# Kernel optimization log

Hardware: AMD Instinct MI355X
Metric: run time of the kernel (lower is better)

The kernel has to match this reference:

```python
import jax, jax.numpy as jnp
import numpy as np

EPS = 1e-8  # torch cosine_similarity norm clamp
TEMP = 1.0

def _gelu(h):
    return jax.nn.gelu(h, approximate=False)  # torch nn.GELU default (erf)

def _layernorm(h, g, b, eps=1e-5):
    mu = jnp.mean(h, axis=-1, keepdims=True)
    var = jnp.var(h, axis=-1, keepdims=True)
    return (h - mu) * jax.lax.rsqrt(var + eps) * g + b

def _encoder(h, eW1, eb1, eW2, eb2, eW3, eb3, ln_g, ln_b):
    h = _gelu(h @ eW1 + eb1)
    h = _gelu(h @ eW2 + eb2)
    h = h @ eW3 + eb3
    return _layernorm(h, ln_g, ln_b)

def _normalize(v):
    n = jnp.sqrt(jnp.sum(v * v, axis=-1, keepdims=True))
    return v / jnp.maximum(n, EPS)

def setup_inputs() -> dict:
    key = jax.random.key(0)
    ks = jax.random.split(key, 8)
    B, D, H, K = 16384, 512, 512, 11
    s = 0.02
    return {
        'x': jax.random.normal(ks[0], (B, D), jnp.float32),
        'tW1': jax.random.normal(ks[1], (K, D, H), jnp.float32) * s,
        'tb1': jnp.zeros((K, H), jnp.float32),
        'tW2': jax.random.normal(ks[2], (K, H, H), jnp.float32) * s,
        'tb2': jnp.zeros((K, H), jnp.float32),
        'tW3': jax.random.normal(ks[3], (K, H, D), jnp.float32) * s,
        'tb3': jnp.zeros((K, D), jnp.float32),
        'eW1': jax.random.normal(ks[4], (D, H), jnp.float32) * s,
        'eb1': jnp.zeros((H,), jnp.float32),
        'eW2': jax.random.normal(ks[5], (H, H), jnp.float32) * s,
        'eb2': jnp.zeros((H,), jnp.float32),
        'eW3': jax.random.normal(ks[6], (H, H), jnp.float32) * s,
        'eb3': jnp.zeros((H,), jnp.float32),
        'ln_g': jnp.ones((H,), jnp.float32),
        'ln_b': jnp.zeros((H,), jnp.float32),
    }

def reference(x, tW1, tb1, tW2, tb2, tW3, tb3, eW1, eb1, eW2, eb2, eW3, eb3, ln_g, ln_b):
    K = tW1.shape[0]
    # K learned transforms, vectorized over k: [K, B, D]
    h = _gelu(jnp.einsum('bi,kij->kbj', x, tW1) + tb1[:, None, :])
    h = _gelu(jnp.einsum('kbi,kij->kbj', h, tW2) + tb2[:, None, :])
    tx = jnp.einsum('kbi,kij->kbj', h, tW3) + tb3[:, None, :]
    # shared encoder on x and on each transformed view
    z = _encoder(x, eW1, eb1, eW2, eb2, eW3, eb3, ln_g, ln_b)      # [B, H]
    zk = _encoder(tx, eW1, eb1, eW2, eb2, eW3, eb3, ln_g, ln_b)    # [K, B, H]
    zn = _normalize(z)
    zkn = _normalize(zk)
    pos = jnp.einsum('bh,kbh->kb', zn, zkn) / TEMP                 # sim(z, z_k)
    S = jnp.einsum('lbh,kbh->lkb', zkn, zkn) / TEMP                # sim(z_l, z_k)
    diag = jnp.eye(K, dtype=bool)[:, :, None]
    Sm = jnp.where(diag, -jnp.inf, S)                              # drop l == k
    all_terms = jnp.concatenate([pos[None], Sm], axis=0)           # [K+1, K, B]
    log_den = jax.nn.logsumexp(all_terms, axis=0)                  # [K, B]
    return -jnp.sum(pos - log_den, axis=0)                         # [B]
```

## Files before the change

### kernel.cpp

```cpp
#include <hip/hip_runtime.h>
#include <hip/hip_bf16.h>
#include <cstdint>

typedef __attribute__((ext_vector_type(8))) short short8;
typedef __attribute__((ext_vector_type(4))) float f32x4;
typedef __attribute__((ext_vector_type(4))) short short4v;

__device__ __forceinline__ float b2f(short s) {
    unsigned u = ((unsigned)(unsigned short)s) << 16;
    return __builtin_bit_cast(float, u);
}
__device__ __forceinline__ short f2b(float f) {
    unsigned u = __builtin_bit_cast(unsigned, f);
    u += 0x7fff + ((u >> 16) & 1);
    return (short)(u >> 16);
}

__device__ __forceinline__ float gelu_t(float x) {
    const float c1 = 2.302184829f;
    const float c2 = 0.102947246f;
    float x2 = x * x;
    float t  = __builtin_fmaf(c2, x2, c1);
    float e  = __builtin_amdgcn_exp2f(x * t);
    return x - __fdividef(x, e + 1.0f);
}

__device__ __forceinline__ void async16(const void* g, void* l) {
    __builtin_amdgcn_global_load_lds(
        (const __attribute__((address_space(1))) unsigned int*)g,
        (__attribute__((address_space(3))) unsigned int*)l, 16, 0, 0);
}

#define NT 8

template<bool GELU>
__global__ __launch_bounds__(512, 2)
void gemm_bt(const short* __restrict__ A, long sA,
             const short* __restrict__ Bt, long sB,
             const float* __restrict__ bias, long sBias,
             short* __restrict__ C, long sC) {
    const int z = blockIdx.z;
    A    += (long)z * sA;
    Bt   += (long)z * sB;
    bias += (long)z * sBias;
    C    += (long)z * sC;

    const int nwg = (int)gridDim.x;
    const int bx  = (int)blockIdx.x;
    int flat = bx;
    if ((nwg & 7) == 0) { const int q = nwg >> 3; flat = (bx & 7) * q + (bx >> 3); }
    const long arow0 = (long)(flat >> 1) * 256;
    const long brow0 = (long)(flat & 1) * 256;

    __shared__ alignas(16) short smem[2 * 2 * 256 * 64];

    const int tid  = threadIdx.x;
    const int lane = tid & 63;
    const int w    = tid >> 6;
    const int wrow = w >> 2, wcol = w & 3;
    const int lr = lane & 15, hi = lane >> 4;

    f32x4 acc[8][4] = {};

    const int srow = lane >> 3;
    const int sc   = ((lane & 7) ^ srow) * 8;

    auto stage = [&](int q, int t) {
        short* Ab = smem + q * 32768;
        short* Bb = Ab + 16384;
        const int k0 = t * 64;
#pragma unroll
        for (int j = 0; j < 4; ++j) {
            const int rbase = j * 64 + w * 8;
            async16(A  + (arow0 + rbase + srow) * 512 + k0 + sc, Ab + rbase * 64);
            async16(Bt + (brow0 + rbase + srow) * 512 + k0 + sc, Bb + rbase * 64);
        }
    };

    stage(0, 0);

    int buf = 0;
#pragma unroll
    for (int t = 0; t < NT; ++t) {
        if (t + 1 < NT) {
            stage(buf ^ 1, t + 1);
            asm volatile("s_waitcnt vmcnt(8)" ::: "memory");
        } else {
            asm volatile("s_waitcnt vmcnt(0)" ::: "memory");
        }
        __builtin_amdgcn_sched_barrier(0);
        __builtin_amdgcn_s_barrier();
        __builtin_amdgcn_sched_barrier(0);

        const short* Ab = smem + buf * 32768;
        const short* Bb = Ab + 16384;
#pragma unroll
        for (int ks = 0; ks < 2; ++ks) {
            const int ch = ks * 4 + hi;
            short8 a[8], b[4];
#pragma unroll
            for (int n = 0; n < 4; ++n) {
                const int r = wcol * 64 + n * 16 + lr;
                b[n] = *(const short8*)&Bb[r * 64 + ((ch ^ (r & 7)) * 8)];
            }
#pragma unroll
            for (int m = 0; m < 8; ++m) {
                const int r = wrow * 128 + m * 16 + lr;
                a[m] = *(const short8*)&Ab[r * 64 + ((ch ^ (r & 7)) * 8)];
            }
            __builtin_amdgcn_s_setprio(1);
#pragma unroll
            for (int m = 0; m < 8; ++m)
#pragma unroll
                for (int n = 0; n < 4; ++n)
                    acc[m][n] = __builtin_amdgcn_mfma_f32_16x16x32_bf16(
                        a[m], b[n], acc[m][n], 0, 0, 0);
            __builtin_amdgcn_s_setprio(0);
        }

        __builtin_amdgcn_s_barrier();
        buf ^= 1;
    }

    short* E = smem + w * (32 * 72);
    const int cl = lr, rl = hi * 4;
#pragma unroll
    for (int h = 0; h < 4; ++h) {
#pragma unroll
        for (int n = 0; n < 4; ++n) {
            const int col = (int)brow0 + wcol * 64 + n * 16 + cl;
            const float bs = bias[col];
            const int ecol = n * 16 + cl;
#pragma unroll
            for (int ml = 0; ml < 2; ++ml) {
                const int m = h * 2 + ml;
                float g0 = acc[m][n][0] + bs, g1 = acc[m][n][1] + bs;
                float g2 = acc[m][n][2] + bs, g3 = acc[m][n][3] + bs;
                if (GELU) { g0 = gelu_t(g0); g1 = gelu_t(g1); g2 = gelu_t(g2); g3 = gelu_t(g3); }
                unsigned p01, p23;
                asm("v_cvt_pk_bf16_f32 %0, %1, %2" : "=v"(p01) : "v"(g0), "v"(g1));
                asm("v_cvt_pk_bf16_f32 %0, %1, %2" : "=v"(p23) : "v"(g2), "v"(g3));
                const int r0 = ml * 16 + rl;
                E[(r0 + 0) * 72 + ecol] = (short)(p01 & 0xffff);
                E[(r0 + 1) * 72 + ecol] = (short)(p01 >> 16);
                E[(r0 + 2) * 72 + ecol] = (short)(p23 & 0xffff);
                E[(r0 + 3) * 72 + ecol] = (short)(p23 >> 16);
            }
        }
#pragma unroll
        for (int chunk = 0; chunk < 4; ++chunk) {
            const int rloc = chunk * 8 + (lane >> 3);
            const int c0   = (lane & 7) * 8;
            short8 v = *(const short8*)&E[rloc * 72 + c0];
            *(short8*)&C[(arow0 + wrow * 128 + h * 32 + rloc) * 512
                         + brow0 + wcol * 64 + c0] = v;
        }
    }
}

__global__ __launch_bounds__(256)
void transpose_conv(const float* __restrict__ src, short* __restrict__ dst) {
    __shared__ float t[32][33];
    const long moff = (long)blockIdx.z * 512 * 512;
    const float* s = src + moff;
    short* d = dst + moff;
    const int tx = threadIdx.x & 31, ty = threadIdx.x >> 5;
    const int bi = blockIdx.x, bj = blockIdx.y;
#pragma unroll
    for (int j = 0; j < 4; ++j)
        t[ty + j * 8][tx] = s[(long)(bi * 32 + ty + j * 8) * 512 + bj * 32 + tx];
    __syncthreads();
#pragma unroll
    for (int j = 0; j < 4; ++j)
        d[(long)(bj * 32 + ty + j * 8) * 512 + bi * 32 + tx] = f2b(t[tx][ty + j * 8]);
}

__global__ __launch_bounds__(256)
void conv_f32_bf16_2(const float* __restrict__ src, short* __restrict__ d1,
                     short* __restrict__ d2, long n) {
    long i = ((long)blockIdx.x * 256 + threadIdx.x) * 4;
    if (i >= n) return;
    float4 f = *(const float4*)&src[i];
    short4v o;
    o[0] = f2b(f.x); o[1] = f2b(f.y); o[2] = f2b(f.z); o[3] = f2b(f.w);
    *(short4v*)&d1[i] = o;
    *(short4v*)&d2[i] = o;
}

__global__ __launch_bounds__(256)
void ln_loss(const short* __restrict__ H, const float* __restrict__ g,
             const float* __restrict__ bta, float* __restrict__ out, int CH) {
    __shared__ alignas(16) short Z[4][16 * 520];
    const int wid = threadIdx.x >> 6, lane = threadIdx.x & 63;
    const long b = (long)blockIdx.x * 4 + wid;
    short* Zw = &Z[wid][0];

#pragma unroll
    for (int r = 12; r < 16; ++r)
        *(short8*)&Zw[r * 520 + lane * 8] = (short8){0, 0, 0, 0, 0, 0, 0, 0};

    for (int s = 0; s < 12; ++s) {
        short8 t = *(const short8*)&H[((long)s * CH + b) * 512 + lane * 8];
        float v[8];
        float sum = 0.f, ss = 0.f;
#pragma unroll
        for (int j = 0; j < 8; ++j) { v[j] = b2f(t[j]); sum += v[j]; ss += v[j] * v[j]; }
#pragma unroll
        for (int o = 1; o < 64; o <<= 1) { sum += __shfl_xor(sum, o, 64); ss += __shfl_xor(ss, o, 64); }
        const float mu = sum * (1.f / 512.f);
        const float rs = rsqrtf(ss * (1.f / 512.f) - mu * mu + 1e-5f);
        float y[8]; float nsq = 0.f;
#pragma unroll
        for (int j = 0; j < 8; ++j) {
            const int col = lane * 8 + j;
            y[j] = (v[j] - mu) * rs * g[col] + bta[col];
            nsq += y[j] * y[j];
        }
#pragma unroll
        for (int o = 1; o < 64; o <<= 1) nsq += __shfl_xor(nsq, o, 64);
        const float inv = 1.f / fmaxf(sqrtf(nsq), 1e-8f);
        short8 o8;
#pragma unroll
        for (int j = 0; j < 8; ++j) o8[j] = f2b(y[j] * inv);
        *(short8*)&Zw[s * 520 + lane * 8] = o8;
    }

    f32x4 acc = {0.f, 0.f, 0.f, 0.f};
    const int lr = lane & 15, hi = lane >> 4;
#pragma unroll
    for (int st = 0; st < 16; ++st) {
        short8 a = *(const short8*)&Zw[lr * 520 + st * 32 + hi * 8];
        acc = __builtin_amdgcn_mfma_f32_16x16x32_bf16(a, a, acc, 0, 0, 0);
    }
    const int col = lr;
    float lmax = -3.0e38f;
    bool valid[4];
#pragma unroll
    for (int i = 0; i < 4; ++i) {
        const int row = hi * 4 + i;
        valid[i] = (row < 12) && (row != col);
        if (valid[i]) lmax = fmaxf(lmax, acc[i]);
    }
    lmax = fmaxf(lmax, __shfl_xor(lmax, 16, 64));
    lmax = fmaxf(lmax, __shfl_xor(lmax, 32, 64));
    float esum = 0.f;
#pragma unroll
    for (int i = 0; i < 4; ++i)
        if (valid[i]) esum += __builtin_amdgcn_exp2f((acc[i] - lmax) * 1.44269504f);
    esum += __shfl_xor(esum, 16, 64);
    esum += __shfl_xor(esum, 32, 64);
    float contrib = 0.f;
    if (hi == 0 && col >= 1 && col <= 11) {
        const float logden = lmax + __builtin_amdgcn_logf(esum) * 0.6931471806f;
        contrib = acc[0] - logden;
    }
#pragma unroll
    for (int o = 1; o < 16; o <<= 1) contrib += __shfl_xor(contrib, o, 64);
    if (lane == 0) out[b] = -contrib;
}

extern "C" void kernel_launch(void* const* d_in, const int* in_sizes, int n_in,
                              void* d_out, int out_size, void* d_ws, size_t ws_size,
                              hipStream_t stream) {
    const float* x    = (const float*)d_in[0];
    const float* tW1  = (const float*)d_in[1];
    const float* tb1  = (const float*)d_in[2];
    const float* tW2  = (const float*)d_in[3];
    const float* tb2  = (const float*)d_in[4];
    const float* tW3  = (const float*)d_in[5];
    const float* tb3  = (const float*)d_in[6];
    const float* eW1  = (const float*)d_in[7];
    const float* eb1  = (const float*)d_in[8];
    const float* eW2  = (const float*)d_in[9];
    const float* eb2  = (const float*)d_in[10];
    const float* eW3  = (const float*)d_in[11];
    const float* eb3  = (const float*)d_in[12];
    const float* ln_g = (const float*)d_in[13];
    const float* ln_b = (const float*)d_in[14];

    const int  B    = in_sizes[0] / 512;
    const long WMAT = 512L * 512L;

    int  c  = 1;
    long CH = B;
    for (;;) {
        CH = (long)B / c;
        size_t need = (size_t)36 * WMAT * 2 + (size_t)24 * CH * 512 * 2 + 4096;
        if (need <= ws_size || CH <= 256) break;
        c <<= 1;
    }
    const long SLAB = 12L * CH * 512;

    short* wt  = (short*)d_ws;
    short* X12 = wt  + 36L * WMAT;
    short* hA  = X12 + SLAB;

    {
        dim3 tgK(16, 16, 11), tg1(16, 16, 1);
        transpose_conv<<<tgK, 256, 0, stream>>>(tW1, wt + 0L * WMAT);
        transpose_conv<<<tgK, 256, 0, stream>>>(tW2, wt + 11L * WMAT);
        transpose_conv<<<tgK, 256, 0, stream>>>(tW3, wt + 22L * WMAT);
        transpose_conv<<<tg1, 256, 0, stream>>>(eW1, wt + 33L * WMAT);
        transpose_conv<<<tg1, 256, 0, stream>>>(eW2, wt + 34L * WMAT);
        transpose_conv<<<tg1, 256, 0, stream>>>(eW3, wt + 35L * WMAT);
    }

    const long SC = CH * 512;
    const dim3 gT((unsigned)(CH / 256 * 2), 1, 11);
    const dim3 gE((unsigned)(12 * CH / 256 * 2), 1, 1);

    for (int ch = 0; ch < c; ++ch) {
        conv_f32_bf16_2<<<(unsigned)((SC / 4 + 255) / 256), 256, 0, stream>>>(
            x + (long)ch * SC, X12, hA, SC);

        gemm_bt<true ><<<gT, 512, 0, stream>>>(hA,        0,  wt + 0L * WMAT,  WMAT, tb1, 512, X12 + SC, SC);
        gemm_bt<true ><<<gT, 512, 0, stream>>>(X12 + SC,  SC, wt + 11L * WMAT, WMAT, tb2, 512, hA + SC,  SC);
        gemm_bt<false><<<gT, 512, 0, stream>>>(hA + SC,   SC, wt + 22L * WMAT, WMAT, tb3, 512, X12 + SC, SC);

        gemm_bt<true ><<<gE, 512, 0, stream>>>(X12, 0, wt + 33L * WMAT, 0, eb1, 0, hA,  0);
        gemm_bt<true ><<<gE, 512, 0, stream>>>(hA,  0, wt + 34L * WMAT, 0, eb2, 0, X12, 0);
        gemm_bt<false><<<gE, 512, 0, stream>>>(X12, 0, wt + 35L * WMAT, 0, eb3, 0, hA,  0);

        ln_loss<<<(unsigned)(CH / 4), 256, 0, stream>>>(
            hA, ln_g, ln_b, (float*)d_out + (long)ch * CH, (int)CH);
    }
}
```

Before: 1.001 ms.

## Fold transform layer-3 weights into encoder first layer to drop a GEMM

Precomputes the products tW3[k]·eW1 (and folded biases tb3·eW1+eb1) once per call, so the third transform GEMM and the first encoder GEMM merge into one batched GEMM over 12 slices. The x slice uses eW1 directly, with a zero-stride first-row arrangement. This removes one full B×512×512×12 GEMM pass and its intermediate traffic, at the cost of small setup GEMMs and extra bf16 rounding of the fused weight matrices.

Measured after the change: 911.2 us. 8.9% less time.

```diff
diff --git a/kernel.cpp b/kernel.cpp
--- a/kernel.cpp
+++ b/kernel.cpp
@@ -176,15 +176,29 @@
 }
 
 __global__ __launch_bounds__(256)
-void conv_f32_bf16_2(const float* __restrict__ src, short* __restrict__ d1,
-                     short* __restrict__ d2, long n) {
+void conv_f32_bf16(const float* __restrict__ src, short* __restrict__ dst, long n) {
     long i = ((long)blockIdx.x * 256 + threadIdx.x) * 4;
     if (i >= n) return;
     float4 f = *(const float4*)&src[i];
     short4v o;
     o[0] = f2b(f.x); o[1] = f2b(f.y); o[2] = f2b(f.z); o[3] = f2b(f.w);
-    *(short4v*)&d1[i] = o;
-    *(short4v*)&d2[i] = o;
+    *(short4v*)&dst[i] = o;
+}
+
+__global__ __launch_bounds__(256)
+void bias_fold(const float* __restrict__ tb3, const short* __restrict__ wtE1,
+               const float* __restrict__ eb1, float* __restrict__ bB) {
+    const int wid = threadIdx.x >> 6, lane = threadIdx.x & 63;
+    const int idx = blockIdx.x * 4 + wid;
+    const int k = idx >> 9, n = idx & 511;
+    short8 wv = *(const short8*)&wtE1[(long)n * 512 + lane * 8];
+    const float* tb = tb3 + (long)k * 512 + lane * 8;
+    float s = 0.f;
+#pragma unroll
+    for (int j = 0; j < 8; ++j) s += b2f(wv[j]) * tb[j];
+#pragma unroll
+    for (int o = 1; o < 64; o <<= 1) s += __shfl_xor(s, o, 64);
+    if (lane == 0) bB[(long)(k + 1) * 512 + n] = s + eb1[n];
 }
 
 __global__ __launch_bounds__(256)
@@ -285,43 +299,56 @@
     long CH = B;
     for (;;) {
         CH = (long)B / c;
-        size_t need = (size_t)36 * WMAT * 2 + (size_t)24 * CH * 512 * 2 + 4096;
+        size_t need = (size_t)48 * WMAT * 2 + (512 + 12 * 512) * 4
+                    + (size_t)24 * CH * 512 * 2 + 8192;
         if (need <= ws_size || CH <= 256) break;
         c <<= 1;
     }
     const long SLAB = 12L * CH * 512;
 
-    short* wt  = (short*)d_ws;
-    short* X12 = wt  + 36L * WMAT;
-    short* hA  = X12 + SLAB;
+    short* wt   = (short*)d_ws;
+    short* Mt   = wt + 36L * WMAT;
+    float* zero512 = (float*)(Mt + 12L * WMAT);
+    float* bB   = zero512 + 512;
+    short* S    = (short*)(bB + 12 * 512);
+    short* T    = S + SLAB;
 
     {
         dim3 tgK(16, 16, 11), tg1(16, 16, 1);
         transpose_conv<<<tgK, 256, 0, stream>>>(tW1, wt + 0L * WMAT);
         transpose_conv<<<tgK, 256, 0, stream>>>(tW2, wt + 11L * WMAT);
-        transpose_conv<<<tgK, 256, 0, stream>>>(tW3, wt + 22L * WMAT);
+        conv_f32_bf16<<<(unsigned)((11 * WMAT / 4 + 255) / 256), 256, 0, stream>>>(
+            tW3, wt + 22L * WMAT, 11 * WMAT);
         transpose_conv<<<tg1, 256, 0, stream>>>(eW1, wt + 33L * WMAT);
         transpose_conv<<<tg1, 256, 0, stream>>>(eW2, wt + 34L * WMAT);
         transpose_conv<<<tg1, 256, 0, stream>>>(eW3, wt + 35L * WMAT);
+
+        hipMemsetAsync(zero512, 0, 512 * sizeof(float), stream);
+        gemm_bt<false><<<dim3(4, 1, 11), 512, 0, stream>>>(
+            wt + 33L * WMAT, 0, wt + 22L * WMAT, WMAT, zero512, 0, Mt + WMAT, WMAT);
+        hipMemcpyAsync(Mt, wt + 33L * WMAT, WMAT * sizeof(short),
+                       hipMemcpyDeviceToDevice, stream);
+        hipMemcpyAsync(bB, eb1, 512 * sizeof(float),
+                       hipMemcpyDeviceToDevice, stream);
+        bias_fold<<<(11 * 512) / 4, 256, 0, stream>>>(tb3, wt + 33L * WMAT, eb1, bB);
     }
 
     const long SC = CH * 512;
     const dim3 gT((unsigned)(CH / 256 * 2), 1, 11);
+    const dim3 gF((unsigned)(CH / 256 * 2), 1, 12);
     const dim3 gE((unsigned)(12 * CH / 256 * 2), 1, 1);
 
     for (int ch = 0; ch < c; ++ch) {
-        conv_f32_bf16_2<<<(unsigned)((SC / 4 + 255) / 256), 256, 0, stream>>>(
-            x + (long)ch * SC, X12, hA, SC);
-
-        gemm_bt<true ><<<gT, 512, 0, stream>>>(hA,        0,  wt + 0L * WMAT,  WMAT, tb1, 512, X12 + SC, SC);
-        gemm_bt<true ><<<gT, 512, 0, stream>>>(X12 + SC,  SC, wt + 11L * WMAT, WMAT, tb2, 512, hA + SC,  SC);
-        gemm_bt<false><<<gT, 512, 0, stream>>>(hA + SC,   SC, wt + 22L * WMAT, WMAT, tb3, 512, X12 + SC, SC);
-
-        gemm_bt<true ><<<gE, 512, 0, stream>>>(X12, 0, wt + 33L * WMAT, 0, eb1, 0, hA,  0);
-        gemm_bt<true ><<<gE, 512, 0, stream>>>(hA,  0, wt + 34L * WMAT, 0, eb2, 0, X12, 0);
-        gemm_bt<false><<<gE, 512, 0, stream>>>(X12, 0, wt + 35L * WMAT, 0, eb3, 0, hA,  0);
+        conv_f32_bf16<<<(unsigned)((SC / 4 + 255) / 256), 256, 0, stream>>>(
+            x + (long)ch * SC, S, SC);
+
+        gemm_bt<true ><<<gT, 512, 0, stream>>>(S, 0,  wt + 0L * WMAT,  WMAT, tb1, 512, T + SC, SC);
+        gemm_bt<true ><<<gT, 512, 0, stream>>>(T + SC, SC, wt + 11L * WMAT, WMAT, tb2, 512, S + SC, SC);
+        gemm_bt<true ><<<gF, 512, 0, stream>>>(S, SC, Mt, WMAT, bB, 512, T, SC);
+        gemm_bt<true ><<<gE, 512, 0, stream>>>(T, 0, wt + 34L * WMAT, 0, eb2, 0, S, 0);
+        gemm_bt<false><<<gE, 512, 0, stream>>>(S, 0, wt + 35L * WMAT, 0, eb3, 0, T, 0);
 
         ln_loss<<<(unsigned)(CH / 4), 256, 0, stream>>>(
-            hA, ln_g, ln_b, (float*)d_out + (long)ch * CH, (int)CH);
-    }
-}
+            T, ln_g, ln_b, (float*)d_out + (long)ch * CH, (int)CH);
+    }
+}
```
